# Kernel optimization log

Hardware: AMD Instinct MI355X
Metric: run time of the kernel (lower is better)

The kernel has to match this reference:

```python
import jax, jax.numpy as jnp
import numpy as np

DIM = 768
NUM_HEADS = 12
HEAD_DIM = DIM // NUM_HEADS
SCALE = HEAD_DIM ** -0.5


def setup_inputs() -> dict:
    key = jax.random.key(0)
    ks = jax.random.split(key, 6)
    B, Lq, Lkv = 8, 1024, 1024
    return {
        "q": jax.random.normal(ks[0], (B, Lq, DIM), dtype=jnp.float32),
        "kv": jax.random.normal(ks[1], (B, Lkv, DIM), dtype=jnp.float32),
        "attn_pos": jax.random.normal(ks[2], (1, NUM_HEADS, Lq, Lkv), dtype=jnp.float32),
        "Wq": jax.random.normal(ks[3], (DIM, DIM), dtype=jnp.float32) * (DIM ** -0.5),
        "Wkv": jax.random.normal(ks[4], (2 * DIM, DIM), dtype=jnp.float32) * (DIM ** -0.5),
        "Wproj": jax.random.normal(ks[5], (DIM, DIM), dtype=jnp.float32) * (DIM ** -0.5),
        "bproj": jnp.zeros((DIM,), dtype=jnp.float32),
    }


def reference(q, kv, attn_pos, Wq, Wkv, Wproj, bproj):
    B, Lq, C = q.shape
    Lkv = kv.shape[1]
    H, D = NUM_HEADS, HEAD_DIM
    # q/kv projections (torch Linear: x @ W.T); attn_pos_encoding_only path
    qh = (q @ Wq.T).reshape(B, Lq, H, D).transpose(0, 2, 1, 3)        # (B,H,Lq,D)
    kvp = (kv @ Wkv.T).reshape(B, Lkv, 2, H, D).transpose(2, 0, 3, 1, 4)
    k, v = kvp[0], kvp[1]                                             # (B,H,Lkv,D)
    # scaled dot-product attention with additive positional bias
    attn = jnp.einsum('bhqd,bhkd->bhqk', qh, k) * SCALE + attn_pos    # (B,H,Lq,Lkv)
    attn = jax.nn.softmax(attn, axis=-1)
    x = jnp.einsum('bhqk,bhkd->bhqd', attn, v)                        # (B,H,Lq,D)
    x = x.transpose(0, 2, 1, 3).reshape(B, Lq, C)
    return x @ Wproj.T + bproj
```

## Files before the change

kernel.cpp:

```cpp
#include <hip/hip_runtime.h>

#define DIM 768
#define NHEADS 12
#define HDIM 64
#define BATCH 8
#define LQ 1024
#define LKV 1024
#define ATTN_SCALE 0.125f
#define LOG2E 1.4426950408889634f
#define C1_SL2E 0.18033688011112042f

typedef __bf16 bf16;
typedef __bf16 bf16x4 __attribute__((ext_vector_type(4)));
typedef __bf16 bf16x8 __attribute__((ext_vector_type(8)));
typedef short s16x4 __attribute__((ext_vector_type(4)));
typedef float f32x4 __attribute__((ext_vector_type(4)));

union B4 { bf16x4 h; s16x4 s; };

static __device__ __forceinline__ f32x4 mfma_k32(bf16x8 a, bf16x8 b, f32x4 c) {
    return __builtin_amdgcn_mfma_f32_16x16x32_bf16(a, b, c, 0, 0, 0);
}
static __device__ __forceinline__ f32x4 mfma_k16(s16x4 a, s16x4 b, f32x4 c) {
    return __builtin_amdgcn_mfma_f32_16x16x16bf16_1k(a, b, c, 0, 0, 0);
}

static __device__ __forceinline__ void async16(const bf16* g, bf16* l) {
    __builtin_amdgcn_global_load_lds(
        (const __attribute__((address_space(1))) unsigned int*)g,
        (__attribute__((address_space(3))) unsigned int*)l, 16, 0, 0);
}
static __device__ __forceinline__ void drain_vmem() {
    __asm__ volatile("s_waitcnt vmcnt(0)" ::: "memory");
}
#define WAIT_VMCNT(N) __asm__ volatile("s_waitcnt vmcnt(" #N ")" ::: "memory")
static __device__ __forceinline__ void code_fence() {
    __asm__ volatile("" ::: "memory");
}

#define NQ4 (BATCH * LQ * DIM / 4)
#define NW4 (DIM * DIM / 4)
__global__ void cvt_all(const float4* __restrict__ q, const float4* __restrict__ kv,
                        const float4* __restrict__ Wq, const float4* __restrict__ Wkv,
                        const float4* __restrict__ Wp,
                        bf16x4* __restrict__ qb, bf16x4* __restrict__ kvb,
                        bf16x4* __restrict__ wall, bf16x4* __restrict__ wpb) {
    int i = blockIdx.x * 256 + threadIdx.x;
    const float4* src; bf16x4* dst; int j;
    if (i < NQ4)                { src = q;   dst = qb;        j = i; }
    else if (i < 2 * NQ4)       { src = kv;  dst = kvb;       j = i - NQ4; }
    else if (i < 2 * NQ4 + NW4) { src = Wq;  dst = wall;      j = i - 2 * NQ4; }
    else if (i < 2 * NQ4 + 3 * NW4) { src = Wkv; dst = wall + NW4; j = i - 2 * NQ4 - NW4; }
    else if (i < 2 * NQ4 + 4 * NW4) { src = Wp;  dst = wpb;   j = i - 2 * NQ4 - 3 * NW4; }
    else return;
    float4 v = src[j];
    bf16x4 o;
    o[0] = (bf16)v.x; o[1] = (bf16)v.y; o[2] = (bf16)v.z; o[3] = (bf16)v.w;
    dst[j] = o;
}

__global__ __launch_bounds__(256) void proj_gemm(
    const bf16* __restrict__ qb, const bf16* __restrict__ kvb,
    const bf16* __restrict__ W,
    bf16* __restrict__ Qp, bf16* __restrict__ Kp, bf16* __restrict__ Vt)
{
    __shared__ bf16 As[128 * 64];
    __shared__ bf16 Bs[128 * 64];
    const int tid  = threadIdx.x;
    const int lane = tid & 63;
    const int w    = tid >> 6;
    const int wm = (w >> 1) * 64;
    const int wn = (w & 1) * 64;
    const int m0 = blockIdx.x * 128;
    const int n0 = blockIdx.y * 128;
    const int K = DIM;
    const int lq = lane & 15;
    const int quad = lane >> 4;

    const bf16* A = (n0 < DIM) ? qb : kvb;
    const int isV = (n0 >= 2 * DIM);

    const int rl8 = lane >> 3;
    const int ch  = lane & 7;
    const int swc = (ch ^ rl8) * 8;
    const bf16* gA = A + (size_t)(m0 + w * 32 + rl8) * K + swc;
    const bf16* gB = W + (size_t)(n0 + w * 32 + rl8) * K + swc;
    bf16* lA = &As[w * 2048];
    bf16* lB = &Bs[w * 2048];

    f32x4 acc[4][4] = {};

    for (int k0 = 0; k0 < K; k0 += 64) {
        #pragma unroll
        for (int p = 0; p < 4; p++) {
            async16(gA + (size_t)(p * 8) * K + k0, lA + p * 512);
            async16(gB + (size_t)(p * 8) * K + k0, lB + p * 512);
        }
        drain_vmem();
        __syncthreads();

        #pragma unroll
        for (int ki = 0; ki < 2; ki++) {
            bf16x8 a[4], b[4];
            #pragma unroll
            for (int i = 0; i < 4; i++) {
                const int ra = wm + i * 16 + lq;
                a[i] = *(const bf16x8*)&As[ra * 64 + (((ki * 4 + quad) ^ (lq & 7)) * 8)];
            }
            #pragma unroll
            for (int j = 0; j < 4; j++) {
                const int rb = wn + j * 16 + lq;
                b[j] = *(const bf16x8*)&Bs[rb * 64 + (((ki * 4 + quad) ^ (lq & 7)) * 8)];
            }
            if (isV) {
                #pragma unroll
                for (int i = 0; i < 4; i++)
                    #pragma unroll
                    for (int j = 0; j < 4; j++)
                        acc[i][j] = mfma_k32(a[i], b[j], acc[i][j]);
            } else {
                #pragma unroll
                for (int i = 0; i < 4; i++)
                    #pragma unroll
                    for (int j = 0; j < 4; j++)
                        acc[i][j] = mfma_k32(b[j], a[i], acc[i][j]);
            }
        }
        __syncthreads();
    }

    if (isV) {
        const int n0v = n0 - 2 * DIM;
        #pragma unroll
        for (int i = 0; i < 4; i++) {
            const int base_m = m0 + wm + i * 16;
            const int b_idx = base_m >> 10;
            const int kvl = (base_m & 1023) + quad * 4;
            #pragma unroll
            for (int j = 0; j < 4; j++) {
                const int nl = n0v + wn + j * 16 + lq;
                const int h = nl >> 6;
                const int d = nl & 63;
                B4 pk;
                #pragma unroll
                for (int r = 0; r < 4; r++) pk.h[r] = (bf16)acc[i][j][r];
                *(s16x4*)&Vt[(((size_t)b_idx * NHEADS + h) * HDIM + d) * LKV + kvl] = pk.s;
            }
        }
    } else {
        bf16* Cb = (n0 < DIM) ? Qp : Kp;
        const float cs = (n0 < DIM) ? C1_SL2E : 1.0f;
        const int nb = (n0 < DIM) ? n0 : n0 - DIM;
        #pragma unroll
        for (int i = 0; i < 4; i++) {
            const size_t row = m0 + wm + i * 16 + lq;
            #pragma unroll
            for (int j = 0; j < 4; j++) {
                const int col = nb + wn + j * 16 + quad * 4;
                B4 pk;
                #pragma unroll
                for (int r = 0; r < 4; r++) pk.h[r] = (bf16)(acc[i][j][r] * cs);
                *(s16x4*)&Cb[row * DIM + col] = pk.s;
            }
        }
    }
}

__global__ __launch_bounds__(256) void out_gemm(
    const bf16* __restrict__ A, const bf16* __restrict__ B,
    float* __restrict__ Cp, const float* __restrict__ bias, int M, int N, int K)
{
    __shared__ bf16 As[64 * 64];
    __shared__ bf16 Bs[128 * 64];
    const int tid  = threadIdx.x;
    const int lane = tid & 63;
    const int w    = tid >> 6;
    const int wm = (w >> 1) * 32;
    const int wn = (w & 1) * 64;
    const int m0 = blockIdx.x * 64;
    const int n0 = blockIdx.y * 128;
    const int lq = lane & 15;
    const int quad = lane >> 4;

    const int rl8 = lane >> 3;
    const int ch  = lane & 7;
    const int swc = (ch ^ rl8) * 8;
    const bf16* gA = A + (size_t)(m0 + w * 16 + rl8) * K + swc;
    const bf16* gB = B + (size_t)(n0 + w * 32 + rl8) * K + swc;
    bf16* lA = &As[w * 1024];
    bf16* lB = &Bs[w * 2048];

    f32x4 acc[2][4] = {};

    for (int k0 = 0; k0 < K; k0 += 64) {
        #pragma unroll
        for (int p = 0; p < 2; p++)
            async16(gA + (size_t)(p * 8) * K + k0, lA + p * 512);
        #pragma unroll
        for (int p = 0; p < 4; p++)
            async16(gB + (size_t)(p * 8) * K + k0, lB + p * 512);
        drain_vmem();
        __syncthreads();

        #pragma unroll
        for (int ki = 0; ki < 2; ki++) {
            bf16x8 a[2], b[4];
            #pragma unroll
            for (int i = 0; i < 2; i++) {
                const int ra = wm + i * 16 + lq;
                a[i] = *(const bf16x8*)&As[ra * 64 + (((ki * 4 + quad) ^ (lq & 7)) * 8)];
            }
            #pragma unroll
            for (int j = 0; j < 4; j++) {
                const int rb = wn + j * 16 + lq;
                b[j] = *(const bf16x8*)&Bs[rb * 64 + (((ki * 4 + quad) ^ (lq & 7)) * 8)];
            }
            #pragma unroll
            for (int i = 0; i < 2; i++)
                #pragma unroll
                for (int j = 0; j < 4; j++)
                    acc[i][j] = mfma_k32(b[j], a[i], acc[i][j]);
        }
        __syncthreads();
    }

    #pragma unroll
    for (int i = 0; i < 2; i++) {
        const size_t row = m0 + wm + i * 16 + lq;
        #pragma unroll
        for (int j = 0; j < 4; j++) {
            const int col = n0 + wn + j * 16 + quad * 4;
            float4 bj = *(const float4*)&bias[col];
            float4 o;
            o.x = acc[i][j][0] + bj.x; o.y = acc[i][j][1] + bj.y;
            o.z = acc[i][j][2] + bj.z; o.w = acc[i][j][3] + bj.w;
            *(float4*)&Cp[row * N + col] = o;
        }
    }
}

__global__ __launch_bounds__(512) void attn_kernel(
    const bf16* __restrict__ Qb,
    const bf16* __restrict__ Kb,
    const bf16* __restrict__ Vt,
    const float* __restrict__ pos,
    bf16* __restrict__ O)
{
    __shared__ bf16 Ks[2][64 * 64];
    __shared__ bf16 Vs[2][64 * 64];

    const int i  = blockIdx.x;
    const int g  = (i & 7) * 12 + (i >> 6);
    const int b  = (i >> 3) & 7;
    const int h  = g >> 3;
    const int q0 = (g & 7) * 128;
    const int bh = b * NHEADS + h;
    const int t = threadIdx.x;
    const int lane = t & 63;
    const int w = t >> 6;
    const int lq = lane & 15;
    const int quad = lane >> 4;

    const bf16* qg = Qb + (size_t)(b * LQ + q0 + w * 16 + lq) * DIM + h * HDIM + quad * 8;
    bf16x8 qa0 = *(const bf16x8*)(qg);
    bf16x8 qa1 = *(const bf16x8*)(qg + 32);

    const int srow  = t >> 3;
    const int chunk = t & 7;
    const int sw    = (chunk ^ (srow & 7)) * 8;
    const bf16* Kg = Kb + (size_t)(b * LKV + srow) * DIM + h * HDIM + sw;
    const bf16* Vg = Vt + (size_t)(bh * HDIM + srow) * LKV + sw;

#define STAGE(kv0, bufi) do {                                                 \
    async16(Kg + (size_t)(kv0) * DIM, &Ks[bufi][srow * 64 + chunk * 8]);      \
    async16(Vg + (kv0),               &Vs[bufi][srow * 64 + chunk * 8]);      \
} while (0)

#define NT (LKV / 64)

    const float4* pos4 = (const float4*)(pos + ((size_t)h * LQ + q0 + w * 16 + lq) * LKV);

    B4 onesb;
    onesb.s = (s16x4){0x3F80, 0x3F80, 0x3F80, 0x3F80};

    f32x4 o_acc[4] = {};
    f32x4 o_l = {};

    STAGE(0, 0);
    float4 pA0 = pos4[quad],      pA1 = pos4[4 + quad];
    float4 pA2 = pos4[8 + quad],  pA3 = pos4[12 + quad];
    WAIT_VMCNT(4);
    __builtin_amdgcn_s_barrier();
    code_fence();

#define QK(BUF, KB, S) do {                                                                   \
    const int krow = (KB) * 16 + lq;                                                          \
    bf16x8 ak0 = *(const bf16x8*)&Ks[BUF][krow * 64 + ((quad) ^ (lq & 7)) * 8];               \
    bf16x8 ak1 = *(const bf16x8*)&Ks[BUF][krow * 64 + ((4 + quad) ^ (lq & 7)) * 8];           \
    S = mfma_k32(ak0, qa0, (f32x4){0.f, 0.f, 0.f, 0.f});                                      \
    S = mfma_k32(ak1, qa1, S);                                                                \
} while (0)

#define SMB(S, P, PF) do {                                       \
    float p0 = exp2f(fmaf((P).x, LOG2E, (S)[0]));                \
    float p1 = exp2f(fmaf((P).y, LOG2E, (S)[1]));                \
    float p2 = exp2f(fmaf((P).z, LOG2E, (S)[2]));                \
    float p3 = exp2f(fmaf((P).w, LOG2E, (S)[3]));                \
    (PF).h[0] = (bf16)p0; (PF).h[1] = (bf16)p1;                  \
    (PF).h[2] = (bf16)p2; (PF).h[3] = (bf16)p3;                  \
} while (0)

#define BODY(IT, BUF) do {                                                                     \
    if ((IT) + 1 < NT) STAGE(((IT) + 1) * 64, (BUF) ^ 1);                                      \
    const int pbn = ((IT) + 1) * 16 + quad;                                                    \
    B4 pf[4];                                                                                  \
    f32x4 s0, s1, s2, s3;                                                                      \
    __builtin_amdgcn_s_setprio(1);                                                             \
    QK(BUF, 0, s0);                                                                            \
    QK(BUF, 1, s1);                                                                            \
    SMB(s0, pA0, pf[0]); if ((IT) + 1 < NT) pA0 = pos4[pbn];                                   \
    QK(BUF, 2, s2);                                                                            \
    SMB(s1, pA1, pf[1]); if ((IT) + 1 < NT) pA1 = pos4[pbn + 4];                               \
    QK(BUF, 3, s3);                                                                            \
    SMB(s2, pA2, pf[2]); if ((IT) + 1 < NT) pA2 = pos4[pbn + 8];                               \
    SMB(s3, pA3, pf[3]); if ((IT) + 1 < NT) pA3 = pos4[pbn + 12];                              \
    _Pragma("unroll")                                                                          \
    for (int kb = 0; kb < 4; kb++)                                                             \
        o_l = mfma_k16(onesb.s, pf[kb].s, o_l);                                                \
    _Pragma("unroll")                                                                          \
    for (int db = 0; db < 4; db++) {                                                           \
        const int vrow = db * 16 + lq;                                                         \
        _Pragma("unroll")                                                                      \
        for (int kb = 0; kb < 4; kb++) {                                                       \
            s16x4 va = *(const s16x4*)&Vs[BUF][vrow * 64                                       \
                          + (((kb * 2 + (quad >> 1)) ^ (lq & 7)) * 8) + (quad & 1) * 4];       \
            o_acc[db] = mfma_k16(va, pf[kb].s, o_acc[db]);                                     \
        }                                                                                      \
    }                                                                                          \
    __builtin_amdgcn_s_setprio(0);                                                             \
    if ((IT) + 1 < NT) {                                                                       \
        WAIT_VMCNT(4);                           \
        __builtin_amdgcn_s_barrier();                           \
        code_fence();                                  \
    }                                                                                          \
} while (0)

    for (int it2 = 0; it2 < NT; it2 += 2) {
        BODY(it2,     0);
        BODY(it2 + 1, 1);
    }
#undef BODY
#undef SMB
#undef QK
#undef STAGE

    float inv = 1.f / o_l[0];
    const size_t orow = (size_t)(b * LQ + q0 + w * 16 + lq) * DIM + h * HDIM;
    #pragma unroll
    for (int dblk = 0; dblk < 4; dblk++) {
        B4 ob;
        #pragma unroll
        for (int r = 0; r < 4; r++) ob.h[r] = (bf16)(o_acc[dblk][r] * inv);
        *(s16x4*)&O[orow + dblk * 16 + quad * 4] = ob.s;
    }
}

extern "C" void kernel_launch(void* const* d_in, const int* in_sizes, int n_in,
                              void* d_out, int out_size, void* d_ws, size_t ws_size,
                              hipStream_t stream) {
    const float* q     = (const float*)d_in[0];
    const float* kv    = (const float*)d_in[1];
    const float* pos   = (const float*)d_in[2];
    const float* Wq    = (const float*)d_in[3];
    const float* Wkv   = (const float*)d_in[4];
    const float* Wproj = (const float*)d_in[5];
    const float* bproj = (const float*)d_in[6];
    float* out = (float*)d_out;

    char* ws = (char*)d_ws;
    size_t off = 0;
    auto alloc = [&](size_t bytes) -> void* {
        void* p = ws + off;
        off += (bytes + 255) & ~(size_t)255;
        return p;
    };

    const int M = BATCH * LQ;
    bf16* qb   = (bf16*)alloc((size_t)M * DIM * 2);
    bf16* kvb  = (bf16*)alloc((size_t)M * DIM * 2);
    bf16* wall = (bf16*)alloc((size_t)3 * DIM * DIM * 2);
    bf16* wpb  = (bf16*)alloc((size_t)DIM * DIM * 2);
    bf16* Qp   = (bf16*)alloc((size_t)M * DIM * 2);
    bf16* Kp   = (bf16*)alloc((size_t)M * DIM * 2);
    bf16* Vt   = (bf16*)alloc((size_t)BATCH * NHEADS * HDIM * LKV * 2);
    bf16* Ob   = (bf16*)alloc((size_t)M * DIM * 2);

    {
        int total = 2 * NQ4 + 4 * NW4;
        cvt_all<<<(total + 255) / 256, 256, 0, stream>>>(
            (const float4*)q, (const float4*)kv, (const float4*)Wq,
            (const float4*)Wkv, (const float4*)Wproj,
            (bf16x4*)qb, (bf16x4*)kvb, (bf16x4*)wall, (bf16x4*)wpb);
    }

    proj_gemm<<<dim3(M / 128, (3 * DIM) / 128), 256, 0, stream>>>(qb, kvb, wall, Qp, Kp, Vt);
    attn_kernel<<<dim3((LQ / 128) * NHEADS * BATCH), 512, 0, stream>>>(Qp, Kp, Vt, pos, Ob);
    out_gemm<<<dim3(M / 64, DIM / 128), 256, 0, stream>>>(Ob, wpb, out, bproj, M, DIM, DIM);
}
```

Measured before the change: 269.2 us.

## Pre-convert positional bias to scaled fp16 inside projection GEMM, reuse output buffer

The projection GEMM now also streams the fp32 attention positional bias, multiplies it by log2(e), converts it to fp16, and writes it into the output buffer as scratch. This overlaps the bias conversion with the GEMM's async loads. The attention kernel then reads half as many bias bytes per tile and drops one multiply per score. The costs are fp16 precision on the bias, an extra load and store in every GEMM iteration with a relaxed vmcnt wait, and reuse of the output buffer that out_gemm later overwrites.

```diff
diff --git a/kernel.cpp b/kernel.cpp
--- a/kernel.cpp
+++ b/kernel.cpp
@@ -15,6 +15,8 @@
 typedef __bf16 bf16x8 __attribute__((ext_vector_type(8)));
 typedef short s16x4 __attribute__((ext_vector_type(4)));
 typedef float f32x4 __attribute__((ext_vector_type(4)));
+typedef _Float16 f16;
+typedef f16 f16x4 __attribute__((ext_vector_type(4)));
 
 union B4 { bf16x4 h; s16x4 s; };
 
@@ -40,6 +42,7 @@
 
 #define NQ4 (BATCH * LQ * DIM / 4)
 #define NW4 (DIM * DIM / 4)
+#define NP4H (NHEADS * LQ * LKV / 4)
 __global__ void cvt_all(const float4* __restrict__ q, const float4* __restrict__ kv,
                         const float4* __restrict__ Wq, const float4* __restrict__ Wkv,
                         const float4* __restrict__ Wp,
@@ -62,7 +65,8 @@
 __global__ __launch_bounds__(256) void proj_gemm(
     const bf16* __restrict__ qb, const bf16* __restrict__ kvb,
     const bf16* __restrict__ W,
-    bf16* __restrict__ Qp, bf16* __restrict__ Kp, bf16* __restrict__ Vt)
+    bf16* __restrict__ Qp, bf16* __restrict__ Kp, bf16* __restrict__ Vt,
+    const float4* __restrict__ posg, f16x4* __restrict__ posh)
 {
     __shared__ bf16 As[128 * 64];
     __shared__ bf16 Bs[128 * 64];
@@ -88,16 +92,23 @@
     bf16* lA = &As[w * 2048];
     bf16* lB = &Bs[w * 2048];
 
+    const int bid = blockIdx.y * 64 + blockIdx.x;
+    const int slotbase = bid * 12 * 256 + tid;
+
     f32x4 acc[4][4] = {};
 
     for (int k0 = 0; k0 < K; k0 += 64) {
+        const int it = k0 >> 6;
         #pragma unroll
         for (int p = 0; p < 4; p++) {
             async16(gA + (size_t)(p * 8) * K + k0, lA + p * 512);
             async16(gB + (size_t)(p * 8) * K + k0, lB + p * 512);
         }
-        drain_vmem();
-        __syncthreads();
+        const int slot = slotbase + it * 256;
+        float4 pv = posg[slot < NP4H ? slot : (NP4H - 1)];
+        WAIT_VMCNT(1);
+        __builtin_amdgcn_s_barrier();
+        code_fence();
 
         #pragma unroll
         for (int ki = 0; ki < 2; ki++) {
@@ -126,7 +137,15 @@
                         acc[i][j] = mfma_k32(b[j], a[i], acc[i][j]);
             }
         }
-        __syncthreads();
+        __builtin_amdgcn_s_barrier();
+        code_fence();
+
+        if (slot < NP4H) {
+            f16x4 pf;
+            pf[0] = (f16)(pv.x * LOG2E); pf[1] = (f16)(pv.y * LOG2E);
+            pf[2] = (f16)(pv.z * LOG2E); pf[3] = (f16)(pv.w * LOG2E);
+            posh[slot] = pf;
+        }
     }
 
     if (isV) {
@@ -243,7 +262,7 @@
     const bf16* __restrict__ Qb,
     const bf16* __restrict__ Kb,
     const bf16* __restrict__ Vt,
-    const float* __restrict__ pos,
+    const f16*  __restrict__ posh,
     bf16* __restrict__ O)
 {
     __shared__ bf16 Ks[2][64 * 64];
@@ -278,7 +297,7 @@
 
 #define NT (LKV / 64)
 
-    const float4* pos4 = (const float4*)(pos + ((size_t)h * LQ + q0 + w * 16 + lq) * LKV);
+    const f16* pg = posh + ((size_t)h * LQ + q0 + w * 16 + lq) * LKV + quad * 4;
 
     B4 onesb;
     onesb.s = (s16x4){0x3F80, 0x3F80, 0x3F80, 0x3F80};
@@ -287,8 +306,10 @@
     f32x4 o_l = {};
 
     STAGE(0, 0);
-    float4 pA0 = pos4[quad],      pA1 = pos4[4 + quad];
-    float4 pA2 = pos4[8 + quad],  pA3 = pos4[12 + quad];
+    f16x4 pA0 = *(const f16x4*)(pg);
+    f16x4 pA1 = *(const f16x4*)(pg + 16);
+    f16x4 pA2 = *(const f16x4*)(pg + 32);
+    f16x4 pA3 = *(const f16x4*)(pg + 48);
     WAIT_VMCNT(4);
     __builtin_amdgcn_s_barrier();
     code_fence();
@@ -302,28 +323,28 @@
 } while (0)
 
 #define SMB(S, P, PF) do {                                       \
-    float p0 = exp2f(fmaf((P).x, LOG2E, (S)[0]));                \
-    float p1 = exp2f(fmaf((P).y, LOG2E, (S)[1]));                \
-    float p2 = exp2f(fmaf((P).z, LOG2E, (S)[2]));                \
-    float p3 = exp2f(fmaf((P).w, LOG2E, (S)[3]));                \
+    float p0 = exp2f((S)[0] + (float)(P)[0]);                    \
+    float p1 = exp2f((S)[1] + (float)(P)[1]);                    \
+    float p2 = exp2f((S)[2] + (float)(P)[2]);                    \
+    float p3 = exp2f((S)[3] + (float)(P)[3]);                    \
     (PF).h[0] = (bf16)p0; (PF).h[1] = (bf16)p1;                  \
     (PF).h[2] = (bf16)p2; (PF).h[3] = (bf16)p3;                  \
 } while (0)
 
 #define BODY(IT, BUF) do {                                                                     \
     if ((IT) + 1 < NT) STAGE(((IT) + 1) * 64, (BUF) ^ 1);                                      \
-    const int pbn = ((IT) + 1) * 16 + quad;                                                    \
+    const int pbn = ((IT) + 1) * 64;                                                           \
     B4 pf[4];                                                                                  \
     f32x4 s0, s1, s2, s3;                                                                      \
     __builtin_amdgcn_s_setprio(1);                                                             \
     QK(BUF, 0, s0);                                                                            \
     QK(BUF, 1, s1);                                                                            \
-    SMB(s0, pA0, pf[0]); if ((IT) + 1 < NT) pA0 = pos4[pbn];                                   \
+    SMB(s0, pA0, pf[0]); if ((IT) + 1 < NT) pA0 = *(const f16x4*)(pg + pbn);                   \
     QK(BUF, 2, s2);                                                                            \
-    SMB(s1, pA1, pf[1]); if ((IT) + 1 < NT) pA1 = pos4[pbn + 4];                               \
+    SMB(s1, pA1, pf[1]); if ((IT) + 1 < NT) pA1 = *(const f16x4*)(pg + pbn + 16);              \
     QK(BUF, 3, s3);                                                                            \
-    SMB(s2, pA2, pf[2]); if ((IT) + 1 < NT) pA2 = pos4[pbn + 8];                               \
-    SMB(s3, pA3, pf[3]); if ((IT) + 1 < NT) pA3 = pos4[pbn + 12];                              \
+    SMB(s2, pA2, pf[2]); if ((IT) + 1 < NT) pA2 = *(const f16x4*)(pg + pbn + 32);              \
+    SMB(s3, pA3, pf[3]); if ((IT) + 1 < NT) pA3 = *(const f16x4*)(pg + pbn + 48);              \
     _Pragma("unroll")                                                                          \
     for (int kb = 0; kb < 4; kb++)                                                             \
         o_l = mfma_k16(onesb.s, pf[kb].s, o_l);                                                \
@@ -394,6 +415,7 @@
     bf16* Kp   = (bf16*)alloc((size_t)M * DIM * 2);
     bf16* Vt   = (bf16*)alloc((size_t)BATCH * NHEADS * HDIM * LKV * 2);
     bf16* Ob   = (bf16*)alloc((size_t)M * DIM * 2);
+    f16* posh = (f16*)out;
 
     {
         int total = 2 * NQ4 + 4 * NW4;
@@ -403,7 +425,8 @@
             (bf16x4*)qb, (bf16x4*)kvb, (bf16x4*)wall, (bf16x4*)wpb);
     }
 
-    proj_gemm<<<dim3(M / 128, (3 * DIM) / 128), 256, 0, stream>>>(qb, kvb, wall, Qp, Kp, Vt);
-    attn_kernel<<<dim3((LQ / 128) * NHEADS * BATCH), 512, 0, stream>>>(Qp, Kp, Vt, pos, Ob);
+    proj_gemm<<<dim3(M / 128, (3 * DIM) / 128), 256, 0, stream>>>(
+        qb, kvb, wall, Qp, Kp, Vt, (const float4*)pos, (f16x4*)posh);
+    attn_kernel<<<dim3((LQ / 128) * NHEADS * BATCH), 512, 0, stream>>>(Qp, Kp, Vt, posh, Ob);
     out_gemm<<<dim3(M / 64, DIM / 128), 256, 0, stream>>>(Ob, wpb, out, bproj, M, DIM, DIM);
 }
```

Result: slower. 279.7 us (+3.9%).
